# Kernel optimization log

Hardware: AMD Instinct MI355X
Metric: run time of the kernel (lower is better)

The kernel has to match this reference:

```python
import jax, jax.numpy as jnp
import numpy as np

N, E, D, G, L = 100000, 1600000, 32, 64, 3
BN_EPS = 1e-5


def setup_inputs() -> dict:
    key = jax.random.key(0)
    ks = jax.random.split(key, 8)
    x = jax.random.normal(ks[0], (N, D), dtype=jnp.float32)
    edge_index = jax.random.randint(ks[1], (2, E), 0, N, dtype=jnp.int64)
    batch = jnp.sort(jax.random.randint(ks[2], (N,), 0, G, dtype=jnp.int64))
    layer_weights = jnp.ones((L,), dtype=jnp.float32)
    # linears[i]: Linear(D->D) + BN(D) (inference-mode stats) ; L of them
    lin_W = jax.random.normal(ks[3], (L, D, D), dtype=jnp.float32) * (1.0 / np.sqrt(D))
    lin_b = jnp.zeros((L, D), dtype=jnp.float32)
    lin_gamma = jnp.ones((L, D), dtype=jnp.float32)
    lin_beta = jnp.zeros((L, D), dtype=jnp.float32)
    lin_mean = jnp.zeros((L, D), dtype=jnp.float32)
    lin_var = jnp.ones((L, D), dtype=jnp.float32)
    # GINConv MLPs: Linear(D->D) + BN(D) + ELU ; L-1 of them
    conv_W = jax.random.normal(ks[4], (L - 1, D, D), dtype=jnp.float32) * (1.0 / np.sqrt(D))
    conv_b = jnp.zeros((L - 1, D), dtype=jnp.float32)
    conv_gamma = jnp.ones((L - 1, D), dtype=jnp.float32)
    conv_beta = jnp.zeros((L - 1, D), dtype=jnp.float32)
    conv_mean = jnp.zeros((L - 1, D), dtype=jnp.float32)
    conv_var = jnp.ones((L - 1, D), dtype=jnp.float32)
    return {"x": x, "edge_index": edge_index, "batch": batch,
            "layer_weights": layer_weights,
            "lin_W": lin_W, "lin_b": lin_b, "lin_gamma": lin_gamma,
            "lin_beta": lin_beta, "lin_mean": lin_mean, "lin_var": lin_var,
            "conv_W": conv_W, "conv_b": conv_b, "conv_gamma": conv_gamma,
            "conv_beta": conv_beta, "conv_mean": conv_mean, "conv_var": conv_var}


def _mlp(h, W, b, gamma, beta, mean, var):
    # Linear -> BatchNorm1d (inference stats) -> ELU
    h = h @ W + b
    h = (h - mean) * (gamma * jax.lax.rsqrt(var + BN_EPS)) + beta
    return jax.nn.elu(h)


def reference(x, edge_index, batch, layer_weights,
              lin_W, lin_b, lin_gamma, lin_beta, lin_mean, lin_var,
              conv_W, conv_b, conv_gamma, conv_beta, conv_mean, conv_var):
    src, dst = edge_index[0], edge_index[1]
    z = _mlp(x, lin_W[0], lin_b[0], lin_gamma[0], lin_beta[0], lin_mean[0], lin_var[0])
    Z = layer_weights[0] * z
    out = jax.ops.segment_max(z, batch, num_segments=G)  # global_max_pool
    for l in range(1, L):
        # GINConv (eps=0): x' = MLP(x + sum_{j->i} x_j)
        agg = jax.ops.segment_sum(x[src], dst, num_segments=N)
        x = _mlp(x + agg, conv_W[l - 1], conv_b[l - 1], conv_gamma[l - 1],
                 conv_beta[l - 1], conv_mean[l - 1], conv_var[l - 1])
        z = layer_weights[l] * _mlp(x, lin_W[l], lin_b[l], lin_gamma[l],
                                    lin_beta[l], lin_mean[l], lin_var[l])
        Z = Z + z
        out = out + jax.ops.segment_max(z, batch, num_segments=G)
    # dropout p=0.0 is identity
    return (out, Z, x)
```

## Files before the change

### kernel.cpp

```cpp
#include <hip/hip_runtime.h>
#include <math.h>

#define N_NODES 100000
#define N_EDGES 1600000
#define DIM 32
#define N_GROUPS 64
#define BN_EPS 1e-5f

#define BIN_NODES 128
#define NBINS ((N_NODES + BIN_NODES - 1) / BIN_NODES)
#define EPB_HIST 2048
#define HIST_BLOCKS ((N_EDGES + EPB_HIST - 1) / EPB_HIST)
#define EPB_SCAT 8192
#define SCAT_SUB (EPB_SCAT / EPB_HIST)
#define SCAT_BLOCKS ((N_EDGES + EPB_SCAT - 1) / EPB_SCAT)
#define CNT_PAD 16

#define HLS 40

typedef __attribute__((ext_vector_type(8))) short short8;
typedef __attribute__((ext_vector_type(4))) float f32x4;

__device__ __forceinline__ unsigned enc_f32(float f) {
    unsigned u = __float_as_uint(f);
    return (u & 0x80000000u) ? ~u : (u | 0x80000000u);
}
__device__ __forceinline__ float dec_f32(unsigned u) {
    return (u & 0x80000000u) ? __uint_as_float(u & 0x7FFFFFFFu) : __uint_as_float(~u);
}
__device__ __forceinline__ unsigned short f2bf(float f) {
    unsigned u = __float_as_uint(f);
    u += 0x7FFFu + ((u >> 16) & 1u);
    return (unsigned short)(u >> 16);
}

__global__ void fold_kernel(const float* __restrict__ lin_W, const float* __restrict__ lin_b,
                            const float* __restrict__ lin_gamma, const float* __restrict__ lin_beta,
                            const float* __restrict__ lin_mean, const float* __restrict__ lin_var,
                            const float* __restrict__ conv_W, const float* __restrict__ conv_b,
                            const float* __restrict__ conv_gamma, const float* __restrict__ conv_beta,
                            const float* __restrict__ conv_mean, const float* __restrict__ conv_var,
                            float* __restrict__ Wf, float* __restrict__ shf,
                            unsigned short* __restrict__ Wfb,
                            float* __restrict__ out, unsigned* __restrict__ segmx,
                            int* __restrict__ bincnt,
                            unsigned short* __restrict__ x0b,
                            unsigned short* __restrict__ xbufb)
{
    int l = blockIdx.x;
    int t = threadIdx.x;
    if (l == 5) {
        out[t] = 0.f; out[t + 1024] = 0.f;
        segmx[t] = 0; segmx[t + 1024] = 0;
        for (int z = t; z < NBINS * CNT_PAD; z += 1024) bincnt[z] = 0;
        if (t < DIM) {
            x0b[(size_t)N_NODES * DIM + t] = 0;
            xbufb[(size_t)N_NODES * DIM + t] = 0;
        }
        return;
    }
    const float *W, *b, *gm, *bt, *mn, *vr;
    if (l < 3) {
        W = lin_W + l * DIM * DIM; b = lin_b + l * DIM; gm = lin_gamma + l * DIM;
        bt = lin_beta + l * DIM;   mn = lin_mean + l * DIM; vr = lin_var + l * DIM;
    } else {
        int c = l - 3;
        W = conv_W + c * DIM * DIM; b = conv_b + c * DIM; gm = conv_gamma + c * DIM;
        bt = conv_beta + c * DIM;   mn = conv_mean + c * DIM; vr = conv_var + c * DIM;
    }
    int j = t & (DIM - 1);
    float scale = gm[j] / sqrtf(vr[j] + BN_EPS);
    float w = W[t] * scale;
    Wf[l * DIM * DIM + t] = w;
    Wfb[l * DIM * DIM + t] = f2bf(w);
    if (t < DIM) shf[l * DIM + t] = (b[t] - mn[t]) * scale + bt[t];
}

__global__ __launch_bounds__(256) void binhist_kernel(const int* __restrict__ dst,
                                                      int* __restrict__ bincnt,
                                                      int* __restrict__ blockcnt) {
    __shared__ int cnt[NBINS];
    int t = threadIdx.x;
    for (int b = t; b < NBINS; b += 256) cnt[b] = 0;
    __syncthreads();
    int base = blockIdx.x * EPB_HIST;
    for (int i = 0; i < EPB_HIST / 256; ++i) {
        int e = base + i * 256 + t;
        if (e < N_EDGES) atomicAdd(&cnt[dst[e] >> 7], 1);
    }
    __syncthreads();
    for (int b = t; b < NBINS; b += 256) {
        int c = cnt[b];
        blockcnt[(size_t)blockIdx.x * NBINS + b] = c;
        if (c > 0) atomicAdd(&bincnt[b * CNT_PAD], c);
    }
}

__global__ __launch_bounds__(1024) void binscan_kernel(const int* __restrict__ bincnt,
                                                       int* __restrict__ binoff,
                                                       int* __restrict__ bincur) {
    __shared__ int s[1024];
    int t = threadIdx.x;
    int c = (t < NBINS) ? bincnt[t * CNT_PAD] : 0;
    s[t] = c;
    __syncthreads();
    for (int off = 1; off < 1024; off <<= 1) {
        int u = (t >= off) ? s[t - off] : 0;
        __syncthreads();
        s[t] += u;
        __syncthreads();
    }
    if (t < NBINS) { binoff[t] = s[t] - c; bincur[t * CNT_PAD] = s[t] - c; }
    if (t == 0) binoff[NBINS] = N_EDGES;
}

__global__ __launch_bounds__(256) void scatter_linz_kernel(
        const int* __restrict__ src, const int* __restrict__ dst,
        int* __restrict__ bincur, unsigned* __restrict__ binbuf,
        const int* __restrict__ blockcnt,
        const float* __restrict__ x0, unsigned short* __restrict__ x0b,
        const unsigned short* __restrict__ Wb, const float* __restrict__ shfv,
        const int* __restrict__ batch, const float* __restrict__ lw_ptr,
        float* __restrict__ Z, unsigned* __restrict__ segmax)
{
    __shared__ int smem[NBINS];
    int t = threadIdx.x;

    if (blockIdx.x < SCAT_BLOCKS) {
        int* pos = smem;
        for (int b = t; b < NBINS; b += 256) {
            int c = 0;
#pragma unroll
            for (int k = 0; k < SCAT_SUB; ++k) {
                int r = blockIdx.x * SCAT_SUB + k;
                if (r < HIST_BLOCKS) c += blockcnt[(size_t)r * NBINS + b];
            }
            pos[b] = (c > 0) ? atomicAdd(&bincur[b * CNT_PAD], c) : 0;
        }
        __syncthreads();
        int base = blockIdx.x * EPB_SCAT;
        for (int i = 0; i < EPB_SCAT / 256; ++i) {
            int e = base + i * 256 + t;
            if (e < N_EDGES) {
                int d = dst[e];
                int bin = d >> 7;
                int p = atomicAdd(&pos[bin], 1);
                binbuf[p] = ((unsigned)(d & 127) << 17) | (unsigned)src[e];
            }
        }
        return;
    }

    unsigned* segloc = (unsigned*)smem;
    segloc[t] = 0;

    int wv = t >> 6, lane = t & 63;
    int m = lane & 15, kg = lane >> 4;

    short8 b0, b1;
#pragma unroll
    for (int j = 0; j < 8; ++j) {
        int k = kg * 8 + j;
        b0[j] = (short)Wb[k * DIM + m];
        b1[j] = (short)Wb[k * DIM + 16 + m];
    }
    float sh0 = shfv[m], sh1 = shfv[m + 16];
    float lw = lw_ptr[0];
    int blk0 = (blockIdx.x - SCAT_BLOCKS) * 64;
    int gfirst = batch[blk0 < N_NODES ? blk0 : N_NODES - 1];
    int row0 = blk0 + wv * 16;
    __syncthreads();

    if (row0 < N_NODES) {
        const float* rp = x0 + (size_t)(row0 + m) * DIM + kg * 8;
        float4 v0 = *(const float4*)rp;
        float4 v1 = *(const float4*)(rp + 4);
        short8 a;
        a[0] = (short)f2bf(v0.x); a[1] = (short)f2bf(v0.y);
        a[2] = (short)f2bf(v0.z); a[3] = (short)f2bf(v0.w);
        a[4] = (short)f2bf(v1.x); a[5] = (short)f2bf(v1.y);
        a[6] = (short)f2bf(v1.z); a[7] = (short)f2bf(v1.w);
        *(short8*)(x0b + (size_t)(row0 + m) * DIM + kg * 8) = a;

        f32x4 d0 = {0.f, 0.f, 0.f, 0.f}, d1 = {0.f, 0.f, 0.f, 0.f};
        d0 = __builtin_amdgcn_mfma_f32_16x16x32_bf16(a, b0, d0, 0, 0, 0);
        d1 = __builtin_amdgcn_mfma_f32_16x16x32_bf16(a, b1, d1, 0, 0, 0);
#pragma unroll
        for (int r = 0; r < 4; ++r) {
            int row = row0 + kg * 4 + r;
            float a0 = d0[r] + sh0;
            float a1 = d1[r] + sh1;
            float z0 = a0 > 0.f ? a0 : expm1f(a0);
            float z1 = a1 > 0.f ? a1 : expm1f(a1);
            size_t zi = (size_t)row * DIM;
            Z[zi + m] = lw * z0;
            Z[zi + 16 + m] = lw * z1;
            int g = batch[row];
            int go = g - gfirst;
            if (go < 8) {
                atomicMax(&segloc[go * DIM + m], enc_f32(z0));
                atomicMax(&segloc[go * DIM + 16 + m], enc_f32(z1));
            } else {
                atomicMax(&segmax[g * DIM + m], enc_f32(z0));
                atomicMax(&segmax[g * DIM + 16 + m], enc_f32(z1));
            }
        }
    }
    __syncthreads();
    unsigned v = segloc[t];
    if (v) atomicMax(&segmax[(gfirst + (t >> 5)) * DIM + (t & 31)], v);
}

__global__ __launch_bounds__(256) void binsort_kernel(const unsigned* __restrict__ binbuf,
                                                      const int* __restrict__ binoff,
                                                      int* __restrict__ esrc,
                                                      int* __restrict__ nodeptr,
                                                      unsigned* __restrict__ segmax,
                                                      float* __restrict__ out) {
    int t = threadIdx.x;
    if (blockIdx.x >= NBINS) {
        int t2 = (blockIdx.x - NBINS) * 256 + t;
        out[t2] += dec_f32(segmax[t2]);
        segmax[t2] = 0;
        return;
    }
    __shared__ int cnt[BIN_NODES];
    __shared__ int sc[BIN_NODES];
    int bin = blockIdx.x;
    int beg = binoff[bin], end = binoff[bin + 1];
    if (t < BIN_NODES) cnt[t] = 0;
    __syncthreads();
    for (int e = beg + t; e < end; e += 256)
        atomicAdd(&cnt[binbuf[e] >> 17], 1);
    __syncthreads();
    int v = (t < BIN_NODES) ? cnt[t] : 0;
    if (t < BIN_NODES) sc[t] = v;
    __syncthreads();
    for (int off = 1; off < BIN_NODES; off <<= 1) {
        int u = (t < BIN_NODES && t >= off) ? sc[t - off] : 0;
        __syncthreads();
        if (t < BIN_NODES) sc[t] += u;
        __syncthreads();
    }
    if (t < BIN_NODES) {
        int excl = sc[t] - v;
        cnt[t] = excl;
        nodeptr[bin * BIN_NODES + t] = beg + excl;
    }
    __syncthreads();
    for (int e = beg + t; e < end; e += 256) {
        unsigned pe = binbuf[e];
        int dl = (int)(pe >> 17);
        int p = atomicAdd(&cnt[dl], 1);
        esrc[beg + p] = (int)(pe & 0x1FFFFu);
    }
}

#define GIN_FETCH4(I0, A)                                                       \
  {                                                                             \
    _Pragma("unroll")                                                           \
    for (int q_ = 0; q_ < 4; ++q_) {                                            \
      int ii_ = (I0) + q_;                                                      \
      int ei_ = beg + ii_;                                                      \
      ei_ = ei_ < (N_EDGES - 1) ? ei_ : (N_EDGES - 1);                          \
      int s_ = esrc[ei_];                                                       \
      s_ = (ii_ < deg) ? s_ : N_NODES;                                          \
      A[q_] = *(const short8*)(xb + (size_t)s_ * DIM + kg8);                    \
    }                                                                           \
  }

#define GIN_MFMA4(A)                                                            \
  {                                                                             \
    _Pragma("unroll")                                                           \
    for (int q_ = 0; q_ < 4; ++q_) {                                            \
      d0[q_] = __builtin_amdgcn_mfma_f32_16x16x32_bf16(A[q_], bc0, d0[q_], 0, 0, 0); \
      d1[q_] = __builtin_amdgcn_mfma_f32_16x16x32_bf16(A[q_], bc1, d1[q_], 0, 0, 0); \
    }                                                                           \
  }

__global__ __launch_bounds__(256) void gin_fused_kernel(
        const unsigned short* __restrict__ xb,
        const int* __restrict__ esrc,
        const int* __restrict__ nodeptr,
        const unsigned short* __restrict__ Wcb, const float* __restrict__ shc,
        const unsigned short* __restrict__ Wlb, const float* __restrict__ shl,
        const int* __restrict__ batch, const float* __restrict__ lw_ptr,
        unsigned short* __restrict__ xnextb,
        float* __restrict__ xoutf,
        float* __restrict__ Z,
        unsigned* __restrict__ segmax)
{
    __shared__ __align__(16) unsigned short hl[4][16 * HLS];
    __shared__ unsigned segloc[8 * DIM];
    int t = threadIdx.x;
    segloc[t] = 0;

    int wv = t >> 6, lane = t & 63;
    int m = lane & 15, kg = lane >> 4;
    int kg8 = kg * 8;

    short8 bc0, bc1, bl0, bl1;
#pragma unroll
    for (int j = 0; j < 8; ++j) {
        int k = kg8 + j;
        bc0[j] = (short)Wcb[k * DIM + m];
        bc1[j] = (short)Wcb[k * DIM + 16 + m];
        bl0[j] = (short)Wlb[k * DIM + m];
        bl1[j] = (short)Wlb[k * DIM + 16 + m];
    }
    float shc0 = shc[m], shc1 = shc[m + 16];
    float shl0 = shl[m], shl1 = shl[m + 16];
    float lw = lw_ptr[0];
    int blk0 = blockIdx.x * 64;
    int gfirst = batch[blk0 < N_NODES ? blk0 : N_NODES - 1];
    int row0 = blk0 + wv * 16;
    __syncthreads();

    if (row0 < N_NODES) {
        int beg = nodeptr[row0 + m];
        int deg = nodeptr[row0 + m + 1] - beg;
        int md = deg;
#pragma unroll
        for (int off = 1; off < 16; off <<= 1)
            md = max(md, __shfl_xor(md, off, 64));

        short8 aS = *(const short8*)(xb + (size_t)(row0 + m) * DIM + kg8);
        f32x4 d0[4], d1[4];
#pragma unroll
        for (int q = 0; q < 4; ++q) {
            d0[q] = (f32x4){0.f, 0.f, 0.f, 0.f};
            d1[q] = (f32x4){0.f, 0.f, 0.f, 0.f};
        }
        d0[0] = __builtin_amdgcn_mfma_f32_16x16x32_bf16(aS, bc0, d0[0], 0, 0, 0);
        d1[0] = __builtin_amdgcn_mfma_f32_16x16x32_bf16(aS, bc1, d1[0], 0, 0, 0);

        int B = (md + 3) >> 2;
        if (B > 0) {
            short8 aA[4], aB[4];
            GIN_FETCH4(0, aA);
            int k = 1;
            for (; k + 1 < B; k += 2) {
                GIN_FETCH4(4 * k, aB);
                GIN_MFMA4(aA);
                GIN_FETCH4(4 * (k + 1), aA);
                GIN_MFMA4(aB);
            }
            if (k < B) {
                GIN_FETCH4(4 * k, aB);
                GIN_MFMA4(aA);
                GIN_MFMA4(aB);
            } else {
                GIN_MFMA4(aA);
            }
        }

        float hp0[4], hp1[4];
#pragma unroll
        for (int r = 0; r < 4; ++r) {
            float a0 = d0[0][r] + d0[1][r] + d0[2][r] + d0[3][r] + shc0;
            float a1 = d1[0][r] + d1[1][r] + d1[2][r] + d1[3][r] + shc1;
            hp0[r] = a0 > 0.f ? a0 : expm1f(a0);
            hp1[r] = a1 > 0.f ? a1 : expm1f(a1);
        }
#pragma unroll
        for (int r = 0; r < 4; ++r) {
            hl[wv][(kg * 4 + r) * HLS + m] = f2bf(hp0[r]);
            hl[wv][(kg * 4 + r) * HLS + 16 + m] = f2bf(hp1[r]);
        }
        if (xoutf) {
#pragma unroll
            for (int r = 0; r < 4; ++r) {
                int row = row0 + kg * 4 + r;
                xoutf[(size_t)row * DIM + m] = hp0[r];
                xoutf[(size_t)row * DIM + 16 + m] = hp1[r];
            }
        }
        if (xnextb) {
            int ii = lane >> 2, q = lane & 3;
            uint4 pk = *(const uint4*)&hl[wv][ii * HLS + q * 8];
            *(uint4*)(xnextb + (size_t)(row0 + ii) * DIM + q * 8) = pk;
        }

        short8 a2 = *(const short8*)&hl[wv][m * HLS + kg8];
        f32x4 e0 = {0.f, 0.f, 0.f, 0.f}, e1 = {0.f, 0.f, 0.f, 0.f};
        e0 = __builtin_amdgcn_mfma_f32_16x16x32_bf16(a2, bl0, e0, 0, 0, 0);
        e1 = __builtin_amdgcn_mfma_f32_16x16x32_bf16(a2, bl1, e1, 0, 0, 0);
#pragma unroll
        for (int r = 0; r < 4; ++r) {
            int row = row0 + kg * 4 + r;
            float a0 = e0[r] + shl0, a1 = e1[r] + shl1;
            float z0 = a0 > 0.f ? a0 : expm1f(a0);
            float z1 = a1 > 0.f ? a1 : expm1f(a1);
            float zw0 = lw * z0, zw1 = lw * z1;
            size_t zi = (size_t)row * DIM;
            Z[zi + m] += zw0;
            Z[zi + 16 + m] += zw1;
            int g = batch[row];
            int go = g - gfirst;
            if (go < 8) {
                atomicMax(&segloc[go * DIM + m], enc_f32(zw0));
                atomicMax(&segloc[go * DIM + 16 + m], enc_f32(zw1));
            } else {
                atomicMax(&segmax[g * DIM + m], enc_f32(zw0));
                atomicMax(&segmax[g * DIM + 16 + m], enc_f32(zw1));
            }
        }
    }
    __syncthreads();
    unsigned v = segloc[t];
    if (v) atomicMax(&segmax[(gfirst + (t >> 5)) * DIM + (t & 31)], v);
}

__global__ void add_out_kernel(unsigned* __restrict__ segmax, float* __restrict__ out) {
    int t = blockIdx.x * blockDim.x + threadIdx.x;
    out[t] += dec_f32(segmax[t]);
    segmax[t] = 0;
}

extern "C" void kernel_launch(void* const* d_in, const int* in_sizes, int n_in,
                              void* d_out, int out_size, void* d_ws, size_t ws_size,
                              hipStream_t stream) {
    const float* x0        = (const float*)d_in[0];
    const int*   ei        = (const int*)d_in[1];
    const int*   batch     = (const int*)d_in[2];
    const float* lw        = (const float*)d_in[3];
    const float* lin_W     = (const float*)d_in[4];
    const float* lin_b     = (const float*)d_in[5];
    const float* lin_gamma = (const float*)d_in[6];
    const float* lin_beta  = (const float*)d_in[7];
    const float* lin_mean  = (const float*)d_in[8];
    const float* lin_var   = (const float*)d_in[9];
    const float* conv_W    = (const float*)d_in[10];
    const float* conv_b    = (const float*)d_in[11];
    const float* conv_gamma= (const float*)d_in[12];
    const float* conv_beta = (const float*)d_in[13];
    const float* conv_mean = (const float*)d_in[14];
    const float* conv_var  = (const float*)d_in[15];

    float* out  = (float*)d_out;
    float* Z    = out + N_GROUPS * DIM;
    float* xout = Z + (size_t)N_NODES * DIM;

    char* p = (char*)d_ws;
    unsigned short* x0b     = (unsigned short*)p; p += ((size_t)N_NODES * DIM + 8192) * sizeof(unsigned short);
    unsigned short* xbufb   = (unsigned short*)p; p += ((size_t)N_NODES * DIM + 8192) * sizeof(unsigned short);
    unsigned*       binbuf  = (unsigned*)p;       p += (size_t)N_EDGES * sizeof(unsigned);
    int*            esrc    = (int*)p;            p += (size_t)N_EDGES * sizeof(int);
    int*            nodeptr = (int*)p;            p += (NBINS * BIN_NODES + 1) * sizeof(int);
    int*            bincnt  = (int*)p;            p += NBINS * CNT_PAD * sizeof(int);
    int*            binoff  = (int*)p;            p += (NBINS + 1) * sizeof(int);
    int*            bincur  = (int*)p;            p += NBINS * CNT_PAD * sizeof(int);
    unsigned*       segmx   = (unsigned*)p;       p += N_GROUPS * DIM * sizeof(unsigned);
    float*          Wf      = (float*)p;          p += 5 * DIM * DIM * sizeof(float);
    float*          shf     = (float*)p;          p += 5 * DIM * sizeof(float);
    unsigned short* Wfb     = (unsigned short*)p; p += 5 * DIM * DIM * sizeof(unsigned short);

    int* blockcnt = (int*)xbufb;

    const int* src = ei;
    const int* dst = ei + N_EDGES;

    const int gf_blocks = (N_NODES + 63) / 64;

    fold_kernel<<<6, 1024, 0, stream>>>(lin_W, lin_b, lin_gamma, lin_beta, lin_mean, lin_var,
                                        conv_W, conv_b, conv_gamma, conv_beta, conv_mean, conv_var,
                                        Wf, shf, Wfb, out, segmx, bincnt, x0b, xbufb);

    binhist_kernel<<<HIST_BLOCKS, 256, 0, stream>>>(dst, bincnt, blockcnt);
    binscan_kernel<<<1, 1024, 0, stream>>>(bincnt, binoff, bincur);
    scatter_linz_kernel<<<SCAT_BLOCKS + gf_blocks, 256, 0, stream>>>(
        src, dst, bincur, binbuf, blockcnt,
        x0, x0b, Wfb, shf, batch, lw, Z, segmx);
    binsort_kernel<<<NBINS + 8, 256, 0, stream>>>(binbuf, binoff, esrc, nodeptr, segmx, out);

    gin_fused_kernel<<<gf_blocks, 256, 0, stream>>>(x0b, esrc, nodeptr,
                                                    Wfb + 3 * DIM * DIM, shf + 3 * DIM,
                                                    Wfb + 1 * DIM * DIM, shf + 1 * DIM,
                                                    batch, lw + 1,
                                                    xbufb, (float*)nullptr, Z, segmx);
    add_out_kernel<<<8, 256, 0, stream>>>(segmx, out);

    gin_fused_kernel<<<gf_blocks, 256, 0, stream>>>(xbufb, esrc, nodeptr,
                                                    Wfb + 4 * DIM * DIM, shf + 4 * DIM,
                                                    Wfb + 2 * DIM * DIM, shf + 2 * DIM,
                                                    batch, lw + 2,
                                                    (unsigned short*)nullptr, xout, Z, segmx);
    add_out_kernel<<<8, 256, 0, stream>>>(segmx, out);
}
```

Measured before the change: 258.0 us.

## Merge fold with histogram, use per-layer segmax buffers, add nontemporal hints

Folds the weight-folding kernel into the edge histogram launch. Gives each layer its own segment-max buffer, so the intermediate add_out launches and the pooled-output fold inside binsort are replaced by one final add_out3 kernel. Also doubles the scatter/linear block size to 512 threads with 128 nodes per block, and marks many streaming loads and stores as nontemporal. The goal is fewer launches and less cache pollution, at the cost of an added memset and possible changes in occupancy and cache behaviour.

```diff
diff --git a/kernel.cpp b/kernel.cpp
--- a/kernel.cpp
+++ b/kernel.cpp
@@ -14,12 +14,14 @@
 #define EPB_SCAT 8192
 #define SCAT_SUB (EPB_SCAT / EPB_HIST)
 #define SCAT_BLOCKS ((N_EDGES + EPB_SCAT - 1) / EPB_SCAT)
+#define GF2_BLOCKS ((N_NODES + 127) / 128)
 #define CNT_PAD 16
 
 #define HLS 40
 
 typedef __attribute__((ext_vector_type(8))) short short8;
 typedef __attribute__((ext_vector_type(4))) float f32x4;
+typedef __attribute__((ext_vector_type(4))) unsigned u32x4;
 
 __device__ __forceinline__ unsigned enc_f32(float f) {
     unsigned u = __float_as_uint(f);
@@ -34,25 +36,39 @@
     return (unsigned short)(u >> 16);
 }
 
-__global__ void fold_kernel(const float* __restrict__ lin_W, const float* __restrict__ lin_b,
-                            const float* __restrict__ lin_gamma, const float* __restrict__ lin_beta,
-                            const float* __restrict__ lin_mean, const float* __restrict__ lin_var,
-                            const float* __restrict__ conv_W, const float* __restrict__ conv_b,
-                            const float* __restrict__ conv_gamma, const float* __restrict__ conv_beta,
-                            const float* __restrict__ conv_mean, const float* __restrict__ conv_var,
-                            float* __restrict__ Wf, float* __restrict__ shf,
-                            unsigned short* __restrict__ Wfb,
-                            float* __restrict__ out, unsigned* __restrict__ segmx,
-                            int* __restrict__ bincnt,
-                            unsigned short* __restrict__ x0b,
-                            unsigned short* __restrict__ xbufb)
+__global__ __launch_bounds__(256) void foldhist_kernel(
+        const float* __restrict__ lin_W, const float* __restrict__ lin_b,
+        const float* __restrict__ lin_gamma, const float* __restrict__ lin_beta,
+        const float* __restrict__ lin_mean, const float* __restrict__ lin_var,
+        const float* __restrict__ conv_W, const float* __restrict__ conv_b,
+        const float* __restrict__ conv_gamma, const float* __restrict__ conv_beta,
+        const float* __restrict__ conv_mean, const float* __restrict__ conv_var,
+        float* __restrict__ shf, unsigned short* __restrict__ Wfb,
+        unsigned short* __restrict__ x0b, unsigned short* __restrict__ xbufb,
+        const int* __restrict__ dst, int* __restrict__ bincnt,
+        int* __restrict__ blockcnt)
 {
-    int l = blockIdx.x;
+    __shared__ int cnt[NBINS];
+    int bid = blockIdx.x;
     int t = threadIdx.x;
-    if (l == 5) {
-        out[t] = 0.f; out[t + 1024] = 0.f;
-        segmx[t] = 0; segmx[t + 1024] = 0;
-        for (int z = t; z < NBINS * CNT_PAD; z += 1024) bincnt[z] = 0;
+    if (bid >= 6) {
+        int hb = bid - 6;
+        for (int b = t; b < NBINS; b += 256) cnt[b] = 0;
+        __syncthreads();
+        int base = hb * EPB_HIST;
+        for (int i = 0; i < EPB_HIST / 256; ++i) {
+            int e = base + i * 256 + t;
+            if (e < N_EDGES) atomicAdd(&cnt[dst[e] >> 7], 1);
+        }
+        __syncthreads();
+        for (int b = t; b < NBINS; b += 256) {
+            int c = cnt[b];
+            __builtin_nontemporal_store(c, &blockcnt[(size_t)hb * NBINS + b]);
+            if (c > 0) atomicAdd(&bincnt[b * CNT_PAD], c);
+        }
+        return;
+    }
+    if (bid == 5) {
         if (t < DIM) {
             x0b[(size_t)N_NODES * DIM + t] = 0;
             xbufb[(size_t)N_NODES * DIM + t] = 0;
@@ -60,39 +76,22 @@
         return;
     }
     const float *W, *b, *gm, *bt, *mn, *vr;
-    if (l < 3) {
-        W = lin_W + l * DIM * DIM; b = lin_b + l * DIM; gm = lin_gamma + l * DIM;
-        bt = lin_beta + l * DIM;   mn = lin_mean + l * DIM; vr = lin_var + l * DIM;
+    if (bid < 3) {
+        W = lin_W + bid * DIM * DIM; b = lin_b + bid * DIM; gm = lin_gamma + bid * DIM;
+        bt = lin_beta + bid * DIM;   mn = lin_mean + bid * DIM; vr = lin_var + bid * DIM;
     } else {
-        int c = l - 3;
+        int c = bid - 3;
         W = conv_W + c * DIM * DIM; b = conv_b + c * DIM; gm = conv_gamma + c * DIM;
         bt = conv_beta + c * DIM;   mn = conv_mean + c * DIM; vr = conv_var + c * DIM;
     }
-    int j = t & (DIM - 1);
-    float scale = gm[j] / sqrtf(vr[j] + BN_EPS);
-    float w = W[t] * scale;
-    Wf[l * DIM * DIM + t] = w;
-    Wfb[l * DIM * DIM + t] = f2bf(w);
-    if (t < DIM) shf[l * DIM + t] = (b[t] - mn[t]) * scale + bt[t];
-}
-
-__global__ __launch_bounds__(256) void binhist_kernel(const int* __restrict__ dst,
-                                                      int* __restrict__ bincnt,
-                                                      int* __restrict__ blockcnt) {
-    __shared__ int cnt[NBINS];
-    int t = threadIdx.x;
-    for (int b = t; b < NBINS; b += 256) cnt[b] = 0;
-    __syncthreads();
-    int base = blockIdx.x * EPB_HIST;
-    for (int i = 0; i < EPB_HIST / 256; ++i) {
-        int e = base + i * 256 + t;
-        if (e < N_EDGES) atomicAdd(&cnt[dst[e] >> 7], 1);
-    }
-    __syncthreads();
-    for (int b = t; b < NBINS; b += 256) {
-        int c = cnt[b];
-        blockcnt[(size_t)blockIdx.x * NBINS + b] = c;
-        if (c > 0) atomicAdd(&bincnt[b * CNT_PAD], c);
+    for (int idx = t; idx < DIM * DIM; idx += 256) {
+        int j = idx & (DIM - 1);
+        float scale = gm[j] / sqrtf(vr[j] + BN_EPS);
+        Wfb[bid * DIM * DIM + idx] = f2bf(W[idx] * scale);
+    }
+    if (t < DIM) {
+        float scale = gm[t] / sqrtf(vr[t] + BN_EPS);
+        shf[bid * DIM + t] = (b[t] - mn[t]) * scale + bt[t];
     }
 }
 
@@ -114,7 +113,7 @@
     if (t == 0) binoff[NBINS] = N_EDGES;
 }
 
-__global__ __launch_bounds__(256) void scatter_linz_kernel(
+__global__ __launch_bounds__(512) void scatter_linz_kernel(
         const int* __restrict__ src, const int* __restrict__ dst,
         int* __restrict__ bincur, unsigned* __restrict__ binbuf,
         const int* __restrict__ blockcnt,
@@ -128,31 +127,33 @@
 
     if (blockIdx.x < SCAT_BLOCKS) {
         int* pos = smem;
-        for (int b = t; b < NBINS; b += 256) {
+        for (int b = t; b < NBINS; b += 512) {
             int c = 0;
 #pragma unroll
             for (int k = 0; k < SCAT_SUB; ++k) {
                 int r = blockIdx.x * SCAT_SUB + k;
-                if (r < HIST_BLOCKS) c += blockcnt[(size_t)r * NBINS + b];
+                if (r < HIST_BLOCKS)
+                    c += __builtin_nontemporal_load(&blockcnt[(size_t)r * NBINS + b]);
             }
             pos[b] = (c > 0) ? atomicAdd(&bincur[b * CNT_PAD], c) : 0;
         }
         __syncthreads();
         int base = blockIdx.x * EPB_SCAT;
-        for (int i = 0; i < EPB_SCAT / 256; ++i) {
-            int e = base + i * 256 + t;
+        for (int i = 0; i < EPB_SCAT / 512; ++i) {
+            int e = base + i * 512 + t;
             if (e < N_EDGES) {
                 int d = dst[e];
                 int bin = d >> 7;
                 int p = atomicAdd(&pos[bin], 1);
-                binbuf[p] = ((unsigned)(d & 127) << 17) | (unsigned)src[e];
+                unsigned pe = ((unsigned)(d & 127) << 17) | (unsigned)src[e];
+                __builtin_nontemporal_store(pe, &binbuf[p]);
             }
         }
         return;
     }
 
     unsigned* segloc = (unsigned*)smem;
-    segloc[t] = 0;
+    if (t < 8 * DIM) segloc[t] = 0;
 
     int wv = t >> 6, lane = t & 63;
     int m = lane & 15, kg = lane >> 4;
@@ -166,20 +167,20 @@
     }
     float sh0 = shfv[m], sh1 = shfv[m + 16];
     float lw = lw_ptr[0];
-    int blk0 = (blockIdx.x - SCAT_BLOCKS) * 64;
-    int gfirst = batch[blk0 < N_NODES ? blk0 : N_NODES - 1];
+    int blk0 = (blockIdx.x - SCAT_BLOCKS) * 128;
+    int gfirst = batch[blk0];
     int row0 = blk0 + wv * 16;
     __syncthreads();
 
     if (row0 < N_NODES) {
         const float* rp = x0 + (size_t)(row0 + m) * DIM + kg * 8;
-        float4 v0 = *(const float4*)rp;
-        float4 v1 = *(const float4*)(rp + 4);
+        f32x4 v0 = __builtin_nontemporal_load((const f32x4*)rp);
+        f32x4 v1 = __builtin_nontemporal_load((const f32x4*)(rp + 4));
         short8 a;
-        a[0] = (short)f2bf(v0.x); a[1] = (short)f2bf(v0.y);
-        a[2] = (short)f2bf(v0.z); a[3] = (short)f2bf(v0.w);
-        a[4] = (short)f2bf(v1.x); a[5] = (short)f2bf(v1.y);
-        a[6] = (short)f2bf(v1.z); a[7] = (short)f2bf(v1.w);
+        a[0] = (short)f2bf(v0[0]); a[1] = (short)f2bf(v0[1]);
+        a[2] = (short)f2bf(v0[2]); a[3] = (short)f2bf(v0[3]);
+        a[4] = (short)f2bf(v1[0]); a[5] = (short)f2bf(v1[1]);
+        a[6] = (short)f2bf(v1[2]); a[7] = (short)f2bf(v1[3]);
         *(short8*)(x0b + (size_t)(row0 + m) * DIM + kg * 8) = a;
 
         f32x4 d0 = {0.f, 0.f, 0.f, 0.f}, d1 = {0.f, 0.f, 0.f, 0.f};
@@ -193,8 +194,8 @@
             float z0 = a0 > 0.f ? a0 : expm1f(a0);
             float z1 = a1 > 0.f ? a1 : expm1f(a1);
             size_t zi = (size_t)row * DIM;
-            Z[zi + m] = lw * z0;
-            Z[zi + 16 + m] = lw * z1;
+            __builtin_nontemporal_store(lw * z0, &Z[zi + m]);
+            __builtin_nontemporal_store(lw * z1, &Z[zi + 16 + m]);
             int g = batch[row];
             int go = g - gfirst;
             if (go < 8) {
@@ -207,31 +208,25 @@
         }
     }
     __syncthreads();
-    unsigned v = segloc[t];
-    if (v) atomicMax(&segmax[(gfirst + (t >> 5)) * DIM + (t & 31)], v);
+    if (t < 8 * DIM) {
+        unsigned v = segloc[t];
+        if (v) atomicMax(&segmax[(gfirst + (t >> 5)) * DIM + (t & 31)], v);
+    }
 }
 
 __global__ __launch_bounds__(256) void binsort_kernel(const unsigned* __restrict__ binbuf,
                                                       const int* __restrict__ binoff,
                                                       int* __restrict__ esrc,
-                                                      int* __restrict__ nodeptr,
-                                                      unsigned* __restrict__ segmax,
-                                                      float* __restrict__ out) {
-    int t = threadIdx.x;
-    if (blockIdx.x >= NBINS) {
-        int t2 = (blockIdx.x - NBINS) * 256 + t;
-        out[t2] += dec_f32(segmax[t2]);
-        segmax[t2] = 0;
-        return;
-    }
+                                                      int* __restrict__ nodeptr) {
     __shared__ int cnt[BIN_NODES];
     __shared__ int sc[BIN_NODES];
+    int t = threadIdx.x;
     int bin = blockIdx.x;
     int beg = binoff[bin], end = binoff[bin + 1];
     if (t < BIN_NODES) cnt[t] = 0;
     __syncthreads();
     for (int e = beg + t; e < end; e += 256)
-        atomicAdd(&cnt[binbuf[e] >> 17], 1);
+        atomicAdd(&cnt[__builtin_nontemporal_load(&binbuf[e]) >> 17], 1);
     __syncthreads();
     int v = (t < BIN_NODES) ? cnt[t] : 0;
     if (t < BIN_NODES) sc[t] = v;
@@ -249,10 +244,10 @@
     }
     __syncthreads();
     for (int e = beg + t; e < end; e += 256) {
-        unsigned pe = binbuf[e];
+        unsigned pe = __builtin_nontemporal_load(&binbuf[e]);
         int dl = (int)(pe >> 17);
         int p = atomicAdd(&cnt[dl], 1);
-        esrc[beg + p] = (int)(pe & 0x1FFFFu);
+        __builtin_nontemporal_store((int)(pe & 0x1FFFFu), &esrc[beg + p]);
     }
 }
 
@@ -263,7 +258,7 @@
       int ii_ = (I0) + q_;                                                      \
       int ei_ = beg + ii_;                                                      \
       ei_ = ei_ < (N_EDGES - 1) ? ei_ : (N_EDGES - 1);                          \
-      int s_ = esrc[ei_];                                                       \
+      int s_ = __builtin_nontemporal_load(&esrc[ei_]);                          \
       s_ = (ii_ < deg) ? s_ : N_NODES;                                          \
       A[q_] = *(const short8*)(xb + (size_t)s_ * DIM + kg8);                    \
     }                                                                           \
@@ -317,8 +312,8 @@
     __syncthreads();
 
     if (row0 < N_NODES) {
-        int beg = nodeptr[row0 + m];
-        int deg = nodeptr[row0 + m + 1] - beg;
+        int beg = __builtin_nontemporal_load(&nodeptr[row0 + m]);
+        int deg = __builtin_nontemporal_load(&nodeptr[row0 + m + 1]) - beg;
         int md = deg;
 #pragma unroll
         for (int off = 1; off < 16; off <<= 1)
@@ -371,14 +366,14 @@
 #pragma unroll
             for (int r = 0; r < 4; ++r) {
                 int row = row0 + kg * 4 + r;
-                xoutf[(size_t)row * DIM + m] = hp0[r];
-                xoutf[(size_t)row * DIM + 16 + m] = hp1[r];
+                __builtin_nontemporal_store(hp0[r], &xoutf[(size_t)row * DIM + m]);
+                __builtin_nontemporal_store(hp1[r], &xoutf[(size_t)row * DIM + 16 + m]);
             }
         }
         if (xnextb) {
             int ii = lane >> 2, q = lane & 3;
-            uint4 pk = *(const uint4*)&hl[wv][ii * HLS + q * 8];
-            *(uint4*)(xnextb + (size_t)(row0 + ii) * DIM + q * 8) = pk;
+            u32x4 pk = *(const u32x4*)&hl[wv][ii * HLS + q * 8];
+            __builtin_nontemporal_store(pk, (u32x4*)(xnextb + (size_t)(row0 + ii) * DIM + q * 8));
         }
 
         short8 a2 = *(const short8*)&hl[wv][m * HLS + kg8];
@@ -393,8 +388,10 @@
             float z1 = a1 > 0.f ? a1 : expm1f(a1);
             float zw0 = lw * z0, zw1 = lw * z1;
             size_t zi = (size_t)row * DIM;
-            Z[zi + m] += zw0;
-            Z[zi + 16 + m] += zw1;
+            float oz0 = __builtin_nontemporal_load(&Z[zi + m]);
+            float oz1 = __builtin_nontemporal_load(&Z[zi + 16 + m]);
+            __builtin_nontemporal_store(oz0 + zw0, &Z[zi + m]);
+            __builtin_nontemporal_store(oz1 + zw1, &Z[zi + 16 + m]);
             int g = batch[row];
             int go = g - gfirst;
             if (go < 8) {
@@ -411,10 +408,12 @@
     if (v) atomicMax(&segmax[(gfirst + (t >> 5)) * DIM + (t & 31)], v);
 }
 
-__global__ void add_out_kernel(unsigned* __restrict__ segmax, float* __restrict__ out) {
+__global__ void add_out3_kernel(const unsigned* __restrict__ s0,
+                                const unsigned* __restrict__ s1,
+                                const unsigned* __restrict__ s2,
+                                float* __restrict__ out) {
     int t = blockIdx.x * blockDim.x + threadIdx.x;
-    out[t] += dec_f32(segmax[t]);
-    segmax[t] = 0;
+    out[t] = dec_f32(s0[t]) + dec_f32(s1[t]) + dec_f32(s2[t]);
 }
 
 extern "C" void kernel_launch(void* const* d_in, const int* in_sizes, int n_in,
@@ -447,11 +446,10 @@
     unsigned*       binbuf  = (unsigned*)p;       p += (size_t)N_EDGES * sizeof(unsigned);
     int*            esrc    = (int*)p;            p += (size_t)N_EDGES * sizeof(int);
     int*            nodeptr = (int*)p;            p += (NBINS * BIN_NODES + 1) * sizeof(int);
+    unsigned*       segmx   = (unsigned*)p;       p += 3 * N_GROUPS * DIM * sizeof(unsigned);
     int*            bincnt  = (int*)p;            p += NBINS * CNT_PAD * sizeof(int);
     int*            binoff  = (int*)p;            p += (NBINS + 1) * sizeof(int);
     int*            bincur  = (int*)p;            p += NBINS * CNT_PAD * sizeof(int);
-    unsigned*       segmx   = (unsigned*)p;       p += N_GROUPS * DIM * sizeof(unsigned);
-    float*          Wf      = (float*)p;          p += 5 * DIM * DIM * sizeof(float);
     float*          shf     = (float*)p;          p += 5 * DIM * sizeof(float);
     unsigned short* Wfb     = (unsigned short*)p; p += 5 * DIM * DIM * sizeof(unsigned short);
 
@@ -462,28 +460,36 @@
 
     const int gf_blocks = (N_NODES + 63) / 64;
 
-    fold_kernel<<<6, 1024, 0, stream>>>(lin_W, lin_b, lin_gamma, lin_beta, lin_mean, lin_var,
-                                        conv_W, conv_b, conv_gamma, conv_beta, conv_mean, conv_var,
-                                        Wf, shf, Wfb, out, segmx, bincnt, x0b, xbufb);
-
-    binhist_kernel<<<HIST_BLOCKS, 256, 0, stream>>>(dst, bincnt, blockcnt);
+    (void)hipMemsetAsync(segmx, 0,
+                         (3 * N_GROUPS * DIM + NBINS * CNT_PAD) * sizeof(unsigned), stream);
+
+    foldhist_kernel<<<6 + HIST_BLOCKS, 256, 0, stream>>>(
+        lin_W, lin_b, lin_gamma, lin_beta, lin_mean, lin_var,
+        conv_W, conv_b, conv_gamma, conv_beta, conv_mean, conv_var,
+        shf, Wfb, x0b, xbufb, dst, bincnt, blockcnt);
+
     binscan_kernel<<<1, 1024, 0, stream>>>(bincnt, binoff, bincur);
-    scatter_linz_kernel<<<SCAT_BLOCKS + gf_blocks, 256, 0, stream>>>(
+
+    scatter_linz_kernel<<<SCAT_BLOCKS + GF2_BLOCKS, 512, 0, stream>>>(
         src, dst, bincur, binbuf, blockcnt,
         x0, x0b, Wfb, shf, batch, lw, Z, segmx);
-    binsort_kernel<<<NBINS + 8, 256, 0, stream>>>(binbuf, binoff, esrc, nodeptr, segmx, out);
+
+    binsort_kernel<<<NBINS, 256, 0, stream>>>(binbuf, binoff, esrc, nodeptr);
 
     gin_fused_kernel<<<gf_blocks, 256, 0, stream>>>(x0b, esrc, nodeptr,
                                                     Wfb + 3 * DIM * DIM, shf + 3 * DIM,
                                                     Wfb + 1 * DIM * DIM, shf + 1 * DIM,
                                                     batch, lw + 1,
-                                                    xbufb, (float*)nullptr, Z, segmx);
-    add_out_kernel<<<8, 256, 0, stream>>>(segmx, out);
+                                                    xbufb, (float*)nullptr, Z,
+                                                    segmx + N_GROUPS * DIM);
 
     gin_fused_kernel<<<gf_blocks, 256, 0, stream>>>(xbufb, esrc, nodeptr,
                                                     Wfb + 4 * DIM * DIM, shf + 4 * DIM,
                                                     Wfb + 2 * DIM * DIM, shf + 2 * DIM,
                                                     batch, lw + 2,
-                                                    (unsigned short*)nullptr, xout, Z, segmx);
-    add_out_kernel<<<8, 256, 0, stream>>>(segmx, out);
-}
+                                                    (unsigned short*)nullptr, xout, Z,
+                                                    segmx + 2 * N_GROUPS * DIM);
+
+    add_out3_kernel<<<8, 256, 0, stream>>>(segmx, segmx + N_GROUPS * DIM,
+                                           segmx + 2 * N_GROUPS * DIM, out);
+}
```

Measured after the change: 325.4 us. +26.1%, slower.
